# Kernel tuning notes

Hardware: AMD Instinct MI355X
Metric: run time of the kernel (lower is better)

Reference implementation:

```python
import jax, jax.numpy as jnp
import numpy as np

GROUPS = 32
EPS = 1e-5
B, C, H, W = 32, 256, 32, 32


def group_norm(x, scale, bias):
    # x: [B,C,H,W]; GroupNorm over (C//G, H, W) per group
    b, c, h, w = x.shape
    xg = x.reshape(b, GROUPS, c // GROUPS, h, w)
    mu = xg.mean(axis=(2, 3, 4), keepdims=True)
    var = xg.var(axis=(2, 3, 4), keepdims=True)
    xg = (xg - mu) * jax.lax.rsqrt(var + EPS)
    x = xg.reshape(b, c, h, w)
    return x * scale[None, :, None, None] + bias[None, :, None, None]


def tensor_linear(x, Wm, bvec):
    # torch: tensordot(x.permute(0,2,3,1), weight, dims=1) contracts C_in with
    # weight's FIRST axis, i.e. y_d = sum_c x_c * Wm[c, d]
    return jnp.einsum('bchw,cd->bdhw', x, Wm) + bvec[None, :, None, None]


def setup_inputs() -> dict:
    key = jax.random.key(0)
    ks = jax.random.split(key, 6)
    d = {'x': jax.random.normal(ks[0], (B, C, H, W), dtype=jnp.float32)}
    for i, name in enumerate(['q', 'k', 'v', 'o']):
        d[f'W{name}'] = jax.random.normal(ks[1 + i], (C, C), dtype=jnp.float32) * 0.02
        d[f'b{name}'] = jnp.zeros((C,), dtype=jnp.float32)
    for name in ['q', 'k', 'v']:
        d[f'g{name}_s'] = jnp.ones((C,), dtype=jnp.float32)
        d[f'g{name}_b'] = jnp.zeros((C,), dtype=jnp.float32)
    return d


def reference(x, Wq, bq, Wk, bk, Wv, bv, Wo, bo,
              gq_s, gq_b, gk_s, gk_b, gv_s, gv_b):
    b, c, h, w = x.shape
    q = tensor_linear(group_norm(x, gq_s, gq_b), Wq, bq)
    k = tensor_linear(group_norm(x, gk_s, gk_b), Wk, bk)
    v = tensor_linear(group_norm(x, gv_s, gv_b), Wv, bv)
    # full (H*W)x(H*W) attention scores
    att = jnp.einsum('bchw,bcix->bhwix', q, k) * (c ** -0.5)  # [B,H,W,H,W]
    att = jax.nn.softmax(att.reshape(b, h, w, h * w), axis=-1).reshape(b, h, w, h, w)
    hout = jnp.einsum('bhwix,bcix->bchw', att, v)
    return x + tensor_linear(hout, Wo, bo)
```

## Files before the change

### kernel.cpp

```cpp
#include <hip/hip_runtime.h>
#include <stdint.h>


#define NB 32
#define CH 256
#define HWPX 1024

typedef __bf16 bf16x8 __attribute__((ext_vector_type(8)));
typedef float f32x4 __attribute__((ext_vector_type(4)));
typedef float f32x16 __attribute__((ext_vector_type(16)));
typedef unsigned short u16;
typedef unsigned char u8;
typedef unsigned int u32;
typedef u16 u16x8 __attribute__((ext_vector_type(8)));
typedef u32 u32x2 __attribute__((ext_vector_type(2)));

__device__ __forceinline__ u16 f2bf(float f) {
    __bf16 h = (__bf16)f;
    return __builtin_bit_cast(u16, h);
}
__device__ __forceinline__ bf16x8 ldb8(const u16* p) {
    return __builtin_bit_cast(bf16x8, *(const u16x8*)p);
}
__device__ __forceinline__ u32 pkfp8(float a, float b, float c, float d) {
    int w = __builtin_amdgcn_cvt_pk_fp8_f32(a, b, 0, false);
    w = __builtin_amdgcn_cvt_pk_fp8_f32(c, d, w, true);
    return (u32)w;
}
__device__ __forceinline__ void gld_lds16(const u8* g, u8* l) {
    __builtin_amdgcn_global_load_lds(
        (const __attribute__((address_space(1))) void*)g,
        (__attribute__((address_space(3))) void*)l, 16, 0, 0);
}

__global__ __launch_bounds__(256) void wprep(
    const float* __restrict__ Wq, const float* __restrict__ bq,
    const float* __restrict__ gqs, const float* __restrict__ gqb,
    const float* __restrict__ Wk, const float* __restrict__ bk,
    const float* __restrict__ gks, const float* __restrict__ gkb,
    const float* __restrict__ Wv, const float* __restrict__ bv,
    const float* __restrict__ gvs, const float* __restrict__ gvb,
    const float* __restrict__ Wo, const float* __restrict__ bo,
    u16* __restrict__ Wt, float* __restrict__ bias)
{
    int m = blockIdx.x >> 8;
    int d = blockIdx.x & 255;
    int c = threadIdx.x;
    const float *W, *bb, *gs, *gb; float scale;
    const float QSC = 0.09016844005556021f;
    if (m == 0)      { W = Wq; bb = bq; gs = gqs; gb = gqb; scale = QSC; }
    else if (m == 1) { W = Wk; bb = bk; gs = gks; gb = gkb; scale = 1.f; }
    else if (m == 2) { W = Wv; bb = bv; gs = gvs; gb = gvb; scale = 1.f; }
    else             { W = Wo; bb = bo; gs = nullptr; gb = nullptr; scale = 1.f; }
    float w   = W[c * 256 + d];
    float gsc = gs ? gs[c] : 1.f;
    float gbc = gb ? gb[c] : 0.f;
    Wt[((size_t)m << 16) + d * 256 + c] = f2bf(w * gsc * scale);
    __shared__ float red[256];
    red[c] = gbc * w;
    __syncthreads();
    for (int s = 128; s > 0; s >>= 1) { if (c < s) red[c] += red[c + s]; __syncthreads(); }
    if (c == 0) bias[m * 256 + d] = (bb[d] + red[0]) * scale;
}

__global__ __launch_bounds__(256) void gn_kernel(const float* __restrict__ x,
                                                 u16* __restrict__ Xh)
{
    int blk = blockIdx.x;
    int b = blk >> 5, g = blk & 31;
    const float* base = x + (size_t)(b * 256 + g * 8) * 1024;
    int t = threadIdx.x;
    float v[32];
    float s = 0.f, s2 = 0.f;
    #pragma unroll
    for (int j = 0; j < 8; j++) {
        #pragma unroll
        for (int pi = 0; pi < 4; pi++) {
            float val = base[j * 1024 + pi * 256 + t];
            v[j * 4 + pi] = val;
            s += val; s2 += val * val;
        }
    }
    __shared__ float rs[256], rq[256];
    rs[t] = s; rq[t] = s2;
    __syncthreads();
    for (int k = 128; k > 0; k >>= 1) {
        if (t < k) { rs[t] += rs[t + k]; rq[t] += rq[t + k]; }
        __syncthreads();
    }
    float mu  = rs[0] * (1.f / 8192.f);
    float var = rq[0] * (1.f / 8192.f) - mu * mu;
    float rv  = rsqrtf(var + 1e-5f);
    u16* outp = Xh + (size_t)b * (HWPX * CH) + g * 8;
    #pragma unroll
    for (int pi = 0; pi < 4; pi++) {
        int p = pi * 256 + t;
        u16x8 tv;
        #pragma unroll
        for (int j = 0; j < 8; j++) tv[j] = f2bf((v[j * 4 + pi] - mu) * rv);
        *(u16x8*)(outp + (size_t)p * 256) = tv;
    }
}

template <int MODE>
__global__ __launch_bounds__(256) void gemm_nt(
    const u16* __restrict__ A, const u16* __restrict__ Bm,
    const float* __restrict__ bias,
    u8* __restrict__ C8, float* __restrict__ Cf,
    const float* __restrict__ xres)
{
    __shared__ __align__(16) u16 Bt[64 * 256];
    int tid = threadIdx.x;
    int lane = tid & 63, wave = tid >> 6;
    int m0 = blockIdx.y * 64 + wave * 16;
    int n0 = blockIdx.x * 64;

    #pragma unroll
    for (int i = 0; i < 8; i++) {
        int G = i * 256 + tid;
        int row = G >> 5, g = G & 31;
        const u16* src = Bm + (size_t)(n0 + row) * 256 + ((g ^ (row & 7)) << 3);
        gld_lds16((const u8*)src, (u8*)(Bt + (size_t)(i * 256 + wave * 64) * 8));
    }

    int lr = lane & 15, hk = lane >> 4, lk = hk * 8;
    const u16* Ap = A + (size_t)(m0 + lr) * 256 + lk;
    bf16x8 af[8];
    #pragma unroll
    for (int kk = 0; kk < 8; kk++) af[kk] = ldb8(Ap + kk * 32);

    int rowm[4];
    #pragma unroll
    for (int nt = 0; nt < 4; nt++)
        rowm[nt] = (MODE == 0 || MODE == 3) ? (lr * 4 + nt) : (nt * 16 + lr);

    __syncthreads();

    f32x4 acc[4] = {};
    bf16x8 b0[4], b1[4];
    #pragma unroll
    for (int nt = 0; nt < 4; nt++) {
        int g = (0 * 4 + hk) ^ (rowm[nt] & 7);
        b0[nt] = ldb8(Bt + (size_t)(rowm[nt] * 32 + g) * 8);
    }
    #pragma unroll
    for (int kk = 0; kk < 8; kk++) {
        if (kk & 1) {
            if (kk < 7) {
                #pragma unroll
                for (int nt = 0; nt < 4; nt++) {
                    int g = ((kk + 1) * 4 + hk) ^ (rowm[nt] & 7);
                    b0[nt] = ldb8(Bt + (size_t)(rowm[nt] * 32 + g) * 8);
                }
            }
            #pragma unroll
            for (int nt = 0; nt < 4; nt++)
                acc[nt] = __builtin_amdgcn_mfma_f32_16x16x32_bf16(af[kk], b1[nt], acc[nt], 0, 0, 0);
        } else {
            #pragma unroll
            for (int nt = 0; nt < 4; nt++) {
                int g = ((kk + 1) * 4 + hk) ^ (rowm[nt] & 7);
                b1[nt] = ldb8(Bt + (size_t)(rowm[nt] * 32 + g) * 8);
            }
            #pragma unroll
            for (int nt = 0; nt < 4; nt++)
                acc[nt] = __builtin_amdgcn_mfma_f32_16x16x32_bf16(af[kk], b0[nt], acc[nt], 0, 0, 0);
        }
    }
    int rbase = m0 + (hk << 2);
    if (MODE == 0 || MODE == 3) {
        int colbase = n0 + lr * 4;
        #pragma unroll
        for (int j = 0; j < 4; j++) {
            int row = rbase + j;
            u32 w = pkfp8(acc[0][j] + bias[colbase],
                          acc[1][j] + bias[colbase + 1],
                          acc[2][j] + bias[colbase + 2],
                          acc[3][j] + bias[colbase + 3]);
            size_t off;
            if (MODE == 0) {
                off = (size_t)row * 256 + colbase;
            } else {
                off = (size_t)(row >> 10) * 262144 + (size_t)((row & 1023) >> 5) * 8192
                    + (size_t)(colbase >> 4) * 512 + (row & 31) * 16 + (colbase & 15);
            }
            *(u32*)(C8 + off) = w;
        }
    } else {
        #pragma unroll
        for (int nt = 0; nt < 4; nt++) {
            int col = n0 + nt * 16 + lr;
            int b = col >> 10, p = col & 1023;
            #pragma unroll
            for (int j = 0; j < 4; j++) {
                int row = rbase + j;
                float v = acc[nt][j] + bias[row];
                if (MODE == 1) {
                    size_t off = (size_t)b * 262144 + (size_t)(p >> 5) * 8192
                               + (size_t)row * 32 + (p & 31);
                    int w = __builtin_amdgcn_cvt_pk_fp8_f32(v, v, 0, false);
                    C8[off] = (u8)(w & 0xff);
                } else {
                    size_t off = (size_t)b * (CH * HWPX) + (size_t)row * 1024 + p;
                    Cf[off] = v + xres[off];
                }
            }
        }
    }
}

__global__ __launch_bounds__(512, 2) void attn(
    const u8* __restrict__ Qf8, const u8* __restrict__ Kf8,
    const u8* __restrict__ Vf8, u16* __restrict__ O)
{
    __shared__ __align__(16) u8 SM[67584];

    int tid = threadIdx.x;
    int lane = tid & 63, wave = tid >> 6;
    int wq = wave & 3, h = wave >> 2;
    int bid = blockIdx.x;
    int b  = (bid & 7) * 4 + (bid >> 6);
    int qb = (bid >> 3) & 7;
    int q0 = qb * 128 + wq * 32;
    int lq = lane & 31, hi = lane >> 5;

    const u8* Qb = Qf8 + (size_t)b * 262144;
    const u8* Kb = Kf8 + (size_t)b * 262144 + (size_t)h * 131072;
    const u8* Vb = Vf8 + (size_t)b * 262144 + (size_t)h * 131072;

    u8* Kl0 = SM + (size_t)(h * 2) * 8192;
    u8* Kl1 = SM + (size_t)(h * 2 + 1) * 8192;
    u8* Vl0 = SM + 32768 + (size_t)(h * 2) * 8192;
    u8* Vl1 = SM + 32768 + (size_t)(h * 2 + 1) * 8192;
    float* ml = (float*)(SM + 65536);

    long qf[16];
    #pragma unroll
    for (int f = 0; f < 16; f++)
        qf[f] = *(const long*)(Qb + (size_t)(q0 + lq) * 256 + f * 16 + hi * 8);

    f32x16 oa[8] = {};
    float m_run = -1e30f, l_run = 0.f;

    #pragma unroll
    for (int i = 0; i < 2; i++) {
        int Gs = (i * 256 + wq * 64 + lane) << 4;
        int Gd = (i * 256 + wq * 64) << 4;
        gld_lds16(Kb + Gs, Kl0 + Gd);
        gld_lds16(Vb + Gs, Vl0 + Gd);
    }
    __syncthreads();

    for (int t = 0; t < 16; ++t) {
        u8* kcur = (t & 1) ? Kl1 : Kl0;
        u8* vcur = (t & 1) ? Vl1 : Vl0;
        if (t < 15) {
            u8* knxt = (t & 1) ? Kl0 : Kl1;
            u8* vnxt = (t & 1) ? Vl0 : Vl1;
            const u8* ks = Kb + (size_t)(t + 1) * 8192;
            const u8* vs = Vb + (size_t)(t + 1) * 8192;
            #pragma unroll
            for (int i = 0; i < 2; i++) {
                int Gs = (i * 256 + wq * 64 + lane) << 4;
                int Gd = (i * 256 + wq * 64) << 4;
                gld_lds16(ks + Gs, knxt + Gd);
                gld_lds16(vs + Gs, vnxt + Gd);
            }
        }

        f32x16 s0 = {}, s1 = {};
        #pragma unroll
        for (int ff = 0; ff < 8; ff++) {
            long k0 = *(const long*)(kcur + (2 * ff) * 512 + lq * 16 + hi * 8);
            s0 = __builtin_amdgcn_mfma_f32_32x32x16_fp8_fp8(k0, qf[2 * ff], s0, 0, 0, 0);
            long k1 = *(const long*)(kcur + (2 * ff + 1) * 512 + lq * 16 + hi * 8);
            s1 = __builtin_amdgcn_mfma_f32_32x32x16_fp8_fp8(k1, qf[2 * ff + 1], s1, 0, 0, 0);
        }

        long vf[16];
        #pragma unroll
        for (int ct = 0; ct < 8; ct++) {
            vf[2 * ct]     = *(const long*)(vcur + ct * 1024 + lq * 16 + hi * 8);
            vf[2 * ct + 1] = *(const long*)(vcur + ct * 1024 + 512 + lq * 16 + hi * 8);
        }

        float s[16];
        #pragma unroll
        for (int r = 0; r < 16; r++) s[r] = s0[r] + s1[r];

        float m01 = fmaxf(s[0], s[1]),   m23 = fmaxf(s[2], s[3]);
        float m45 = fmaxf(s[4], s[5]),   m67 = fmaxf(s[6], s[7]);
        float m89 = fmaxf(s[8], s[9]),   mab = fmaxf(s[10], s[11]);
        float mcd = fmaxf(s[12], s[13]), mef = fmaxf(s[14], s[15]);
        float mloc = fmaxf(fmaxf(fmaxf(m01, m23), fmaxf(m45, m67)),
                           fmaxf(fmaxf(m89, mab), fmaxf(mcd, mef)));
        if (!__all(mloc - m_run <= 4.f)) {
            float mo = fmaxf(mloc, __shfl_xor(mloc, 32));
            float mn = fmaxf(m_run, mo);
            float sc = exp2f(m_run - mn);
            m_run = mn;
            l_run *= sc;
            #pragma unroll
            for (int ct = 0; ct < 8; ct++) {
                #pragma unroll
                for (int r = 0; r < 16; r++) oa[ct][r] *= sc;
            }
        }
        float p[16];
        #pragma unroll
        for (int r = 0; r < 16; r++) p[r] = exp2f(s[r] - m_run);
        l_run += (((p[0]+p[1])+(p[2]+p[3]))+((p[4]+p[5])+(p[6]+p[7])))
               + (((p[8]+p[9])+(p[10]+p[11]))+((p[12]+p[13])+(p[14]+p[15])));

        u32 a  = pkfp8(p[0],  p[1],  p[2],  p[3]);
        u32 bb = pkfp8(p[4],  p[5],  p[6],  p[7]);
        u32 c  = pkfp8(p[8],  p[9],  p[10], p[11]);
        u32 d  = pkfp8(p[12], p[13], p[14], p[15]);
        u32 xa = (u32)__shfl_xor((int)a, 32),  xb = (u32)__shfl_xor((int)bb, 32);
        u32 xc = (u32)__shfl_xor((int)c, 32),  xd = (u32)__shfl_xor((int)d, 32);
        u32x2 f0 = { hi ? xb : a, hi ? bb : xa };
        u32x2 f1 = { hi ? xd : c, hi ? d  : xc };
        long p0 = __builtin_bit_cast(long, f0);
        long p1 = __builtin_bit_cast(long, f1);

        #pragma unroll
        for (int ct = 0; ct < 8; ct++) {
            oa[ct] = __builtin_amdgcn_mfma_f32_32x32x16_fp8_fp8(vf[2 * ct],     p0, oa[ct], 0, 0, 0);
            oa[ct] = __builtin_amdgcn_mfma_f32_32x32x16_fp8_fp8(vf[2 * ct + 1], p1, oa[ct], 0, 0, 0);
        }
        __syncthreads();
    }

    float lt = l_run + __shfl_xor(l_run, 32);
    if (hi == 0) {
        ml[(wave * 32 + lq) * 2]     = m_run;
        ml[(wave * 32 + lq) * 2 + 1] = lt;
    }
    __syncthreads();
    int pw = wave ^ 4;
    float m_o = ml[(pw * 32 + lq) * 2];
    float l_o = ml[(pw * 32 + lq) * 2 + 1];
    float mm  = fmaxf(m_run, m_o);
    float denom = exp2f(m_run - mm) * lt + exp2f(m_o - mm) * l_o;
    float myw = exp2f(m_run - mm) / denom;
    #pragma unroll
    for (int ct = 0; ct < 8; ct++) {
        #pragma unroll
        for (int r = 0; r < 16; r++) oa[ct][r] *= myw;
    }

    float* mbuf = (float*)SM;
    u16* Ob = O + (size_t)b * (HWPX * CH) + (size_t)(q0 + lq) * 256;
    for (int ch = 0; ch < 2; ++ch) {
        if (h == 1) {
            #pragma unroll
            for (int ctl = 0; ctl < 4; ++ctl) {
                int ct = ch * 4 + ctl;
                #pragma unroll
                for (int r = 0; r < 16; ++r) {
                    int crow = (r & 3) + 8 * (r >> 2) + 4 * hi;
                    mbuf[((wq * 4 + ctl) * 32 + crow) * 32 + lq] = oa[ct][r];
                }
            }
        }
        __syncthreads();
        if (h == 0) {
            #pragma unroll
            for (int ctl = 0; ctl < 4; ++ctl) {
                int ct = ch * 4 + ctl;
                #pragma unroll
                for (int rg = 0; rg < 4; ++rg) {
                    u16* dst = Ob + 32 * ct + 8 * rg + 4 * hi;
                    #pragma unroll
                    for (int v = 0; v < 4; ++v) {
                        int r = rg * 4 + v;
                        int crow = v + 8 * rg + 4 * hi;
                        float sum = oa[ct][r] + mbuf[((wq * 4 + ctl) * 32 + crow) * 32 + lq];
                        dst[v] = f2bf(sum);
                    }
                }
            }
        }
        __syncthreads();
    }
}

extern "C" void kernel_launch(void* const* d_in, const int* in_sizes, int n_in,
                              void* d_out, int out_size, void* d_ws, size_t ws_size,
                              hipStream_t stream)
{
    const float* x   = (const float*)d_in[0];
    const float* Wq  = (const float*)d_in[1];
    const float* bq  = (const float*)d_in[2];
    const float* Wk  = (const float*)d_in[3];
    const float* bk  = (const float*)d_in[4];
    const float* Wv  = (const float*)d_in[5];
    const float* bv  = (const float*)d_in[6];
    const float* Wo  = (const float*)d_in[7];
    const float* bo  = (const float*)d_in[8];
    const float* gqs = (const float*)d_in[9];
    const float* gqb = (const float*)d_in[10];
    const float* gks = (const float*)d_in[11];
    const float* gkb = (const float*)d_in[12];
    const float* gvs = (const float*)d_in[13];
    const float* gvb = (const float*)d_in[14];

    const size_t NEL  = (size_t)NB * HWPX * CH;
    const size_t XHB  = NEL * 2;
    const size_t F8B  = NEL;
    const size_t WTB  = 4 * 65536 * 2;
    const size_t BIASB = 4 * 256 * 4;
    size_t need = XHB + 3 * F8B + WTB + BIASB;
    if (ws_size < need) return;

    char* w = (char*)d_ws;
    u16*  Xh   = (u16*)(w);
    u8*   Qf8  = (u8*)(w + XHB);
    u8*   Kf8  = (u8*)(w + XHB + F8B);
    u8*   Vf8  = (u8*)(w + XHB + 2 * F8B);
    u16*  Wt   = (u16*)(w + XHB + 3 * F8B);
    float* bias = (float*)(w + XHB + 3 * F8B + WTB);

    wprep<<<dim3(1024), dim3(256), 0, stream>>>(Wq, bq, gqs, gqb, Wk, bk, gks, gkb,
                                                Wv, bv, gvs, gvb, Wo, bo, Wt, bias);
    gn_kernel<<<dim3(1024), dim3(256), 0, stream>>>(x, Xh);

    gemm_nt<0><<<dim3(4, 512), dim3(256), 0, stream>>>(Xh, Wt,           bias,       Qf8, nullptr, nullptr);
    gemm_nt<3><<<dim3(4, 512), dim3(256), 0, stream>>>(Xh, Wt + 65536,   bias + 256, Kf8, nullptr, nullptr);
    gemm_nt<1><<<dim3(512, 4), dim3(256), 0, stream>>>(Wt + 131072, Xh,  bias + 512, Vf8, nullptr, nullptr);
    attn<<<dim3(256), dim3(512), 0, stream>>>(Qf8, Kf8, Vf8, Xh);
    gemm_nt<2><<<dim3(512, 4), dim3(256), 0, stream>>>(Wt + 196608, Xh,  bias + 768, nullptr, (float*)d_out, x);
}
```

Measured before the change: 132.4 us.

## Fuse Q/K/V projections into one FP8 GEMM kernel with FP8 normalized input

The group-norm kernel now writes normalized activations as FP8 instead of bf16, and wprep emits FP8 Q/K/V weights (Q scale moved to the epilogue). The three separate bf16 projection GEMMs are replaced by one qkv_gemm launch using 128x128 tiles and FP8 MFMA, writing the Q, K and V layouts directly. The output projection becomes its own kernel. This halves activation bytes, cuts launches and raises math throughput, at the cost of extra quantization error on the normalized input and weights.

After: 116.3 us. 12.2% less time.

```diff
diff --git a/kernel.cpp b/kernel.cpp
--- a/kernel.cpp
+++ b/kernel.cpp
@@ -41,7 +41,7 @@
     const float* __restrict__ Wv, const float* __restrict__ bv,
     const float* __restrict__ gvs, const float* __restrict__ gvb,
     const float* __restrict__ Wo, const float* __restrict__ bo,
-    u16* __restrict__ Wt, float* __restrict__ bias)
+    u16* __restrict__ Wt, u8* __restrict__ W8, float* __restrict__ bias)
 {
     int m = blockIdx.x >> 8;
     int d = blockIdx.x & 255;
@@ -55,7 +55,13 @@
     float w   = W[c * 256 + d];
     float gsc = gs ? gs[c] : 1.f;
     float gbc = gb ? gb[c] : 0.f;
-    Wt[((size_t)m << 16) + d * 256 + c] = f2bf(w * gsc * scale);
+    if (m == 3) {
+        Wt[d * 256 + c] = f2bf(w);
+    } else {
+        float ws = w * gsc;
+        int q = __builtin_amdgcn_cvt_pk_fp8_f32(ws, ws, 0, false);
+        W8[(size_t)(m * 256 + d) * 256 + c] = (u8)(q & 0xff);
+    }
     __shared__ float red[256];
     red[c] = gbc * w;
     __syncthreads();
@@ -64,7 +70,7 @@
 }
 
 __global__ __launch_bounds__(256) void gn_kernel(const float* __restrict__ x,
-                                                 u16* __restrict__ Xh)
+                                                 u8* __restrict__ Xq8)
 {
     int blk = blockIdx.x;
     int b = blk >> 5, g = blk & 31;
@@ -91,118 +97,107 @@
     float mu  = rs[0] * (1.f / 8192.f);
     float var = rq[0] * (1.f / 8192.f) - mu * mu;
     float rv  = rsqrtf(var + 1e-5f);
-    u16* outp = Xh + (size_t)b * (HWPX * CH) + g * 8;
+    u8* outp = Xq8 + (size_t)b * (HWPX * CH) + g * 8;
     #pragma unroll
     for (int pi = 0; pi < 4; pi++) {
         int p = pi * 256 + t;
-        u16x8 tv;
-        #pragma unroll
-        for (int j = 0; j < 8; j++) tv[j] = f2bf((v[j * 4 + pi] - mu) * rv);
-        *(u16x8*)(outp + (size_t)p * 256) = tv;
-    }
-}
-
-template <int MODE>
-__global__ __launch_bounds__(256) void gemm_nt(
-    const u16* __restrict__ A, const u16* __restrict__ Bm,
+        u32 lo = pkfp8((v[0 * 4 + pi] - mu) * rv, (v[1 * 4 + pi] - mu) * rv,
+                       (v[2 * 4 + pi] - mu) * rv, (v[3 * 4 + pi] - mu) * rv);
+        u32 hi = pkfp8((v[4 * 4 + pi] - mu) * rv, (v[5 * 4 + pi] - mu) * rv,
+                       (v[6 * 4 + pi] - mu) * rv, (v[7 * 4 + pi] - mu) * rv);
+        u32x2 pk = { lo, hi };
+        *(u32x2*)(outp + (size_t)p * 256) = pk;
+    }
+}
+
+__global__ __launch_bounds__(256) void qkv_gemm(
+    const u8* __restrict__ X8, const u8* __restrict__ W8,
     const float* __restrict__ bias,
-    u8* __restrict__ C8, float* __restrict__ Cf,
-    const float* __restrict__ xres)
+    u8* __restrict__ Qf8, u8* __restrict__ Kf8, u8* __restrict__ Vf8)
 {
-    __shared__ __align__(16) u16 Bt[64 * 256];
+    __shared__ __align__(16) u8 At[128 * 256];
+    __shared__ __align__(16) u8 Bt[128 * 256];
     int tid = threadIdx.x;
-    int lane = tid & 63, wave = tid >> 6;
-    int m0 = blockIdx.y * 64 + wave * 16;
-    int n0 = blockIdx.x * 64;
-
+    int by = blockIdx.x, bx = blockIdx.y;
+    int mat = bx >> 1, half = bx & 1;
+    int p0 = by * 128;
+
+    const u8* Asrc = X8 + (size_t)p0 * 256;
+    const u8* Bsrc = W8 + (size_t)bx * 128 * 256;
     #pragma unroll
     for (int i = 0; i < 8; i++) {
         int G = i * 256 + tid;
-        int row = G >> 5, g = G & 31;
-        const u16* src = Bm + (size_t)(n0 + row) * 256 + ((g ^ (row & 7)) << 3);
-        gld_lds16((const u8*)src, (u8*)(Bt + (size_t)(i * 256 + wave * 64) * 8));
-    }
-
-    int lr = lane & 15, hk = lane >> 4, lk = hk * 8;
-    const u16* Ap = A + (size_t)(m0 + lr) * 256 + lk;
-    bf16x8 af[8];
-    #pragma unroll
-    for (int kk = 0; kk < 8; kk++) af[kk] = ldb8(Ap + kk * 32);
-
-    int rowm[4];
-    #pragma unroll
-    for (int nt = 0; nt < 4; nt++)
-        rowm[nt] = (MODE == 0 || MODE == 3) ? (lr * 4 + nt) : (nt * 16 + lr);
-
+        int row = G >> 4, g16 = G & 15;
+        int soff = row * 256 + ((g16 ^ (row & 7)) << 4);
+        gld_lds16(Asrc + soff, At + (size_t)G * 16);
+        gld_lds16(Bsrc + soff, Bt + (size_t)G * 16);
+    }
+
+    int lane = tid & 63, w = tid >> 6;
+    int lr = lane & 15, hk = lane >> 4;
+    int sub = (hk & 1) * 8;
     __syncthreads();
 
-    f32x4 acc[4] = {};
-    bf16x8 b0[4], b1[4];
-    #pragma unroll
-    for (int nt = 0; nt < 4; nt++) {
-        int g = (0 * 4 + hk) ^ (rowm[nt] & 7);
-        b0[nt] = ldb8(Bt + (size_t)(rowm[nt] * 32 + g) * 8);
-    }
+    f32x4 acc[2][8] = {};
     #pragma unroll
     for (int kk = 0; kk < 8; kk++) {
-        if (kk & 1) {
-            if (kk < 7) {
+        int g16 = kk * 2 + (hk >> 1);
+        long af[2], bfr[8];
+        #pragma unroll
+        for (int mf = 0; mf < 2; mf++) {
+            int row = w * 32 + mf * 16 + lr;
+            af[mf] = *(const long*)(At + row * 256 + ((g16 ^ (row & 7)) << 4) + sub);
+        }
+        #pragma unroll
+        for (int nt = 0; nt < 8; nt++) {
+            int row = nt * 16 + lr;
+            bfr[nt] = *(const long*)(Bt + row * 256 + ((g16 ^ (row & 7)) << 4) + sub);
+        }
+        #pragma unroll
+        for (int mf = 0; mf < 2; mf++)
+            #pragma unroll
+            for (int nt = 0; nt < 8; nt++)
+                acc[mf][nt] = __builtin_amdgcn_mfma_f32_16x16x32_fp8_fp8(
+                    af[mf], bfr[nt], acc[mf][nt], 0, 0, 0);
+    }
+
+    const float QSC = 0.09016844005556021f;
+    float scale = (mat == 0) ? QSC : 1.f;
+    const float* bs = bias + mat * 256 + half * 128;
+
+    #pragma unroll
+    for (int mf = 0; mf < 2; mf++) {
+        #pragma unroll
+        for (int j = 0; j < 4; j++) {
+            int p = p0 + w * 32 + mf * 16 + (hk << 2) + j;
+            if (mat < 2) {
+                u32 lo = pkfp8(acc[mf][0][j] * scale + bs[0 * 16 + lr],
+                               acc[mf][1][j] * scale + bs[1 * 16 + lr],
+                               acc[mf][2][j] * scale + bs[2 * 16 + lr],
+                               acc[mf][3][j] * scale + bs[3 * 16 + lr]);
+                u32 hi = pkfp8(acc[mf][4][j] * scale + bs[4 * 16 + lr],
+                               acc[mf][5][j] * scale + bs[5 * 16 + lr],
+                               acc[mf][6][j] * scale + bs[6 * 16 + lr],
+                               acc[mf][7][j] * scale + bs[7 * 16 + lr]);
+                u32x2 val = { lo, hi };
+                if (mat == 0) {
+                    *(u32x2*)(Qf8 + (size_t)p * 256 + half * 128 + lr * 8) = val;
+                } else {
+                    int pb = p & 1023;
+                    size_t off = (size_t)(p >> 10) * 262144 + (size_t)(pb >> 5) * 8192
+                               + (size_t)(half * 8 + (lr >> 1)) * 512
+                               + (pb & 31) * 16 + (lr & 1) * 8;
+                    *(u32x2*)(Kf8 + off) = val;
+                }
+            } else {
+                int pb = p & 1023;
+                size_t base = (size_t)(p >> 10) * 262144 + (size_t)(pb >> 5) * 8192 + (pb & 31);
                 #pragma unroll
-                for (int nt = 0; nt < 4; nt++) {
-                    int g = ((kk + 1) * 4 + hk) ^ (rowm[nt] & 7);
-                    b0[nt] = ldb8(Bt + (size_t)(rowm[nt] * 32 + g) * 8);
-                }
-            }
-            #pragma unroll
-            for (int nt = 0; nt < 4; nt++)
-                acc[nt] = __builtin_amdgcn_mfma_f32_16x16x32_bf16(af[kk], b1[nt], acc[nt], 0, 0, 0);
-        } else {
-            #pragma unroll
-            for (int nt = 0; nt < 4; nt++) {
-                int g = ((kk + 1) * 4 + hk) ^ (rowm[nt] & 7);
-                b1[nt] = ldb8(Bt + (size_t)(rowm[nt] * 32 + g) * 8);
-            }
-            #pragma unroll
-            for (int nt = 0; nt < 4; nt++)
-                acc[nt] = __builtin_amdgcn_mfma_f32_16x16x32_bf16(af[kk], b0[nt], acc[nt], 0, 0, 0);
-        }
-    }
-    int rbase = m0 + (hk << 2);
-    if (MODE == 0 || MODE == 3) {
-        int colbase = n0 + lr * 4;
-        #pragma unroll
-        for (int j = 0; j < 4; j++) {
-            int row = rbase + j;
-            u32 w = pkfp8(acc[0][j] + bias[colbase],
-                          acc[1][j] + bias[colbase + 1],
-                          acc[2][j] + bias[colbase + 2],
-                          acc[3][j] + bias[colbase + 3]);
-            size_t off;
-            if (MODE == 0) {
-                off = (size_t)row * 256 + colbase;
-            } else {
-                off = (size_t)(row >> 10) * 262144 + (size_t)((row & 1023) >> 5) * 8192
-                    + (size_t)(colbase >> 4) * 512 + (row & 31) * 16 + (colbase & 15);
-            }
-            *(u32*)(C8 + off) = w;
-        }
-    } else {
-        #pragma unroll
-        for (int nt = 0; nt < 4; nt++) {
-            int col = n0 + nt * 16 + lr;
-            int b = col >> 10, p = col & 1023;
-            #pragma unroll
-            for (int j = 0; j < 4; j++) {
-                int row = rbase + j;
-                float v = acc[nt][j] + bias[row];
-                if (MODE == 1) {
-                    size_t off = (size_t)b * 262144 + (size_t)(p >> 5) * 8192
-                               + (size_t)row * 32 + (p & 31);
-                    int w = __builtin_amdgcn_cvt_pk_fp8_f32(v, v, 0, false);
-                    C8[off] = (u8)(w & 0xff);
-                } else {
-                    size_t off = (size_t)b * (CH * HWPX) + (size_t)row * 1024 + p;
-                    Cf[off] = v + xres[off];
+                for (int nt = 0; nt < 8; nt++) {
+                    int c = half * 128 + nt * 16 + lr;
+                    float vv = acc[mf][nt][j] + bs[nt * 16 + lr];
+                    int q = __builtin_amdgcn_cvt_pk_fp8_f32(vv, vv, 0, false);
+                    Vf8[base + (size_t)c * 32] = (u8)(q & 0xff);
                 }
             }
         }
@@ -382,6 +377,79 @@
             }
         }
         __syncthreads();
+    }
+}
+
+__global__ __launch_bounds__(256) void gemm_out(
+    const u16* __restrict__ A, const u16* __restrict__ Bm,
+    const float* __restrict__ bias,
+    float* __restrict__ Cf, const float* __restrict__ xres)
+{
+    __shared__ __align__(16) u16 Bt[64 * 256];
+    int tid = threadIdx.x;
+    int lane = tid & 63, wave = tid >> 6;
+    int m0 = blockIdx.y * 64 + wave * 16;
+    int n0 = blockIdx.x * 64;
+
+    #pragma unroll
+    for (int i = 0; i < 8; i++) {
+        int G = i * 256 + tid;
+        int row = G >> 5, g = G & 31;
+        const u16* src = Bm + (size_t)(n0 + row) * 256 + ((g ^ (row & 7)) << 3);
+        gld_lds16((const u8*)src, (u8*)(Bt + (size_t)(i * 256 + wave * 64) * 8));
+    }
+
+    int lr = lane & 15, hk = lane >> 4, lk = hk * 8;
+    const u16* Ap = A + (size_t)(m0 + lr) * 256 + lk;
+    bf16x8 af[8];
+    #pragma unroll
+    for (int kk = 0; kk < 8; kk++) af[kk] = ldb8(Ap + kk * 32);
+
+    __syncthreads();
+
+    f32x4 acc[4] = {};
+    bf16x8 b0[4], b1[4];
+    #pragma unroll
+    for (int nt = 0; nt < 4; nt++) {
+        int row = nt * 16 + lr;
+        b0[nt] = ldb8(Bt + (size_t)(row * 32 + (hk ^ (row & 7))) * 8);
+    }
+    #pragma unroll
+    for (int kk = 0; kk < 8; kk++) {
+        if (kk & 1) {
+            if (kk < 7) {
+                #pragma unroll
+                for (int nt = 0; nt < 4; nt++) {
+                    int row = nt * 16 + lr;
+                    b0[nt] = ldb8(Bt + (size_t)(row * 32 + (((kk + 1) * 4 + hk) ^ (row & 7))) * 8);
+                }
+            }
+            #pragma unroll
+            for (int nt = 0; nt < 4; nt++)
+                acc[nt] = __builtin_amdgcn_mfma_f32_16x16x32_bf16(af[kk], b1[nt], acc[nt], 0, 0, 0);
+        } else {
+            #pragma unroll
+            for (int nt = 0; nt < 4; nt++) {
+                int row = nt * 16 + lr;
+                b1[nt] = ldb8(Bt + (size_t)(row * 32 + (((kk + 1) * 4 + hk) ^ (row & 7))) * 8);
+            }
+            #pragma unroll
+            for (int nt = 0; nt < 4; nt++)
+                acc[nt] = __builtin_amdgcn_mfma_f32_16x16x32_bf16(af[kk], b0[nt], acc[nt], 0, 0, 0);
+        }
+    }
+    int rbase = m0 + (hk << 2);
+    #pragma unroll
+    for (int nt = 0; nt < 4; nt++) {
+        int col = n0 + nt * 16 + lr;
+        int b = col >> 10, p = col & 1023;
+        #pragma unroll
+        for (int j = 0; j < 4; j++) {
+            int row = rbase + j;
+            float v = acc[nt][j] + bias[row];
+            size_t off = (size_t)b * (CH * HWPX) + (size_t)row * 1024 + p;
+            Cf[off] = v + xres[off];
+        }
     }
 }
 
@@ -406,28 +474,28 @@
     const float* gvb = (const float*)d_in[14];
 
     const size_t NEL  = (size_t)NB * HWPX * CH;
-    const size_t XHB  = NEL * 2;
     const size_t F8B  = NEL;
-    const size_t WTB  = 4 * 65536 * 2;
+    const size_t OB   = NEL * 2;
+    const size_t WTB  = 65536 * 2;
+    const size_t W8B  = 768 * 256;
     const size_t BIASB = 4 * 256 * 4;
-    size_t need = XHB + 3 * F8B + WTB + BIASB;
+    size_t need = 4 * F8B + OB + WTB + W8B + BIASB;
     if (ws_size < need) return;
 
     char* w = (char*)d_ws;
-    u16*  Xh   = (u16*)(w);
-    u8*   Qf8  = (u8*)(w + XHB);
-    u8*   Kf8  = (u8*)(w + XHB + F8B);
-    u8*   Vf8  = (u8*)(w + XHB + 2 * F8B);
-    u16*  Wt   = (u16*)(w + XHB + 3 * F8B);
-    float* bias = (float*)(w + XHB + 3 * F8B + WTB);
+    u8*   Xq8  = (u8*)(w);
+    u8*   Qf8  = (u8*)(w + F8B);
+    u8*   Kf8  = (u8*)(w + 2 * F8B);
+    u8*   Vf8  = (u8*)(w + 3 * F8B);
+    u16*  O    = (u16*)(w + 4 * F8B);
+    u16*  Wt   = (u16*)(w + 4 * F8B + OB);
+    u8*   W8   = (u8*)(w + 4 * F8B + OB + WTB);
+    float* bias = (float*)(w + 4 * F8B + OB + WTB + W8B);
 
     wprep<<<dim3(1024), dim3(256), 0, stream>>>(Wq, bq, gqs, gqb, Wk, bk, gks, gkb,
-                                                Wv, bv, gvs, gvb, Wo, bo, Wt, bias);
-    gn_kernel<<<dim3(1024), dim3(256), 0, stream>>>(x, Xh);
-
-    gemm_nt<0><<<dim3(4, 512), dim3(256), 0, stream>>>(Xh, Wt,           bias,       Qf8, nullptr, nullptr);
-    gemm_nt<3><<<dim3(4, 512), dim3(256), 0, stream>>>(Xh, Wt + 65536,   bias + 256, Kf8, nullptr, nullptr);
-    gemm_nt<1><<<dim3(512, 4), dim3(256), 0, stream>>>(Wt + 131072, Xh,  bias + 512, Vf8, nullptr, nullptr);
-    attn<<<dim3(256), dim3(512), 0, stream>>>(Qf8, Kf8, Vf8, Xh);
-    gemm_nt<2><<<dim3(512, 4), dim3(256), 0, stream>>>(Wt + 196608, Xh,  bias + 768, nullptr, (float*)d_out, x);
-}
+                                                Wv, bv, gvs, gvb, Wo, bo, Wt, W8, bias);
+    gn_kernel<<<dim3(1024), dim3(256), 0, stream>>>(x, Xq8);
+    qkv_gemm<<<dim3(256, 6), dim3(256), 0, stream>>>(Xq8, W8, bias, Qf8, Kf8, Vf8);
+    attn<<<dim3(256), dim3(512), 0, stream>>>(Qf8, Kf8, Vf8, O);
+    gemm_out<<<dim3(512, 4), dim3(256), 0, stream>>>(Wt, O, bias + 768, (float*)d_out, x);
+}
```
